# Kernel tuning notes

Measured on AMD Instinct MI355X. Metric: run time of the kernel, lower is better.

## Reference

```python
import jax, jax.numpy as jnp
import numpy as np

# config constants (from init_kwargs)
DT = 1.0
TAU_J = 10.0
TAU_M = 20.0
KAPPA_J = 0.25
A_GEN = 1.0
A_DISC = 1.0
THRESH = 0.4
X_DECAY = 20.0  # trace decay constant: x += -x/20 + spikes

B = 8192
LS = [1024, 512, 512, 256]


def setup_inputs() -> dict:
    key = jax.random.key(0)
    ks = jax.random.split(key, 24)
    inp = {}
    inp['x_input'] = (jax.random.uniform(ks[0], (B, LS[0])) < 0.2).astype(jnp.float32)
    inp['y_target'] = (jax.random.uniform(ks[1], (B, LS[3])) < 0.2).astype(jnp.float32)
    # hidden-layer states (layers 1 and 2); layer 0 / last are clamped
    inp['j1'] = jax.random.normal(ks[2], (B, LS[1])) * 0.1
    inp['v1'] = jax.random.normal(ks[3], (B, LS[1])) * 0.1
    inp['s1'] = (jax.random.uniform(ks[4], (B, LS[1])) < 0.2).astype(jnp.float32)
    inp['x1'] = jax.random.uniform(ks[5], (B, LS[1])) * 2.0
    inp['j2'] = jax.random.normal(ks[6], (B, LS[2])) * 0.1
    inp['v2'] = jax.random.normal(ks[7], (B, LS[2])) * 0.1
    inp['s2'] = (jax.random.uniform(ks[8], (B, LS[2])) < 0.2).astype(jnp.float32)
    inp['x2'] = jax.random.uniform(ks[9], (B, LS[2])) * 2.0
    # weights (torch.rand * 0.01)
    inp['W0'] = jax.random.uniform(ks[10], (LS[0], LS[1])) * 0.01
    inp['W1'] = jax.random.uniform(ks[11], (LS[1], LS[2])) * 0.01
    inp['W2'] = jax.random.uniform(ks[12], (LS[2], LS[3])) * 0.01
    inp['V0'] = jax.random.uniform(ks[13], (LS[1], LS[0])) * 0.01
    inp['V1'] = jax.random.uniform(ks[14], (LS[2], LS[1])) * 0.01
    inp['V2'] = jax.random.uniform(ks[15], (LS[3], LS[2])) * 0.01
    inp['Eg0'] = jax.random.uniform(ks[16], (LS[1], LS[0])) * 0.01
    inp['Eg1'] = jax.random.uniform(ks[17], (LS[2], LS[1])) * 0.01
    inp['Eg2'] = jax.random.uniform(ks[18], (LS[3], LS[2])) * 0.01
    inp['Ed0'] = jax.random.uniform(ks[19], (LS[0], LS[1])) * 0.01
    inp['Ed1'] = jax.random.uniform(ks[20], (LS[1], LS[2])) * 0.01
    inp['Ed2'] = jax.random.uniform(ks[21], (LS[2], LS[3])) * 0.01
    return inp


def _lif_update(j, v, x, total_input):
    # Eq 19-24: leaky current integrator -> leaky membrane -> threshold -> reset -> trace
    j = j + (DT / TAU_J) * (-KAPPA_J * j + total_input)
    v = v + (DT / TAU_M) * (-v + j)  # uses updated j, as in the torch code
    spikes = (v > THRESH).astype(v.dtype)
    v = v * (1.0 - spikes)  # hard reset
    x = x + (-x / X_DECAY + spikes)  # spike trace
    return j, v, spikes, x


def reference(x_input, y_target, j1, v1, s1, x1, j2, v2, s2, x2,
              W0, W1, W2, V0, V1, V2, Eg0, Eg1, Eg2, Ed0, Ed1, Ed2):
    # --- phase 1: error neurons (all layers, using current spikes) ---
    # layer 0 clamped: x0 = x_input, s0 = x_input; layer 3 clamped: x3 = s3 = y_target
    e_gen0 = A_GEN * (x_input - s1 @ W0.T)       # [B, 1024]
    e_gen1 = A_GEN * (x1 - s2 @ W1.T)            # [B, 512]
    e_gen2 = A_GEN * (x2 - y_target @ W2.T)      # [B, 512]
    e_disc1 = A_DISC * (x1 - x_input @ V0.T)     # [B, 512]
    e_disc2 = A_DISC * (x2 - s1 @ V1.T)          # [B, 512]
    e_disc3 = A_DISC * (y_target - s2 @ V2.T)    # [B, 256]

    # --- phase 2: value-neuron updates (hidden layers 1 and 2 only) ---
    total1 = -(e_gen1 + e_disc1) + e_gen0 @ Eg0.T + e_disc2 @ Ed1.T
    total2 = -(e_gen2 + e_disc2) + e_gen1 @ Eg1.T + e_disc3 @ Ed2.T

    j1n, v1n, s1n, x1n = _lif_update(j1, v1, x1, total1)
    j2n, v2n, s2n, x2n = _lif_update(j2, v2, x2, total2)

    return jnp.concatenate([j1n, v1n, x1n, s1n, j2n, v2n, x2n, s2n], axis=-1)  # [B, 4096]
```

## Files before the change

### kernel.cpp

```cpp
#include <hip/hip_runtime.h>
#include <stdint.h>
#include <stddef.h>

typedef unsigned short u16;
typedef __attribute__((ext_vector_type(8))) short short8;
typedef __attribute__((ext_vector_type(4))) float f32x4;

#define DEVI __device__ __forceinline__

DEVI u16 f2bf(float f) {
  union { float f; unsigned u; } c; c.f = f;
  unsigned r = c.u + 0x7fff + ((c.u >> 16) & 1);
  return (u16)(r >> 16);
}

DEVI short8 pack8(f32x4 a, f32x4 b) {
  short8 v;
#pragma unroll
  for (int i = 0; i < 4; i++) { v[i] = (short)f2bf(a[i]); v[i + 4] = (short)f2bf(b[i]); }
  return v;
}

typedef __attribute__((address_space(1))) const void global_cvoid;
typedef __attribute__((address_space(3))) void lds_void;

DEVI void mfma_phase(const u16* As, const u16* Bs, f32x4 acc[4][4])
{
  const int lane = threadIdx.x & 63;
  const int w    = threadIdx.x >> 6;
  const int l16  = lane & 15, lq = lane >> 4;
  const int wm   = (w >> 1) * 64, wn = (w & 1) * 64;
#pragma unroll
  for (int kc = 0; kc < 2; kc++) {
    short8 afr[4], bfr[4];
#pragma unroll
    for (int rt = 0; rt < 4; rt++) {
      int m  = wm + rt * 16 + l16;
      int gr = (kc * 4 + lq) ^ (m & 7);
      afr[rt] = *(const short8*)(As + m * 64 + gr * 8);
    }
#pragma unroll
    for (int ct = 0; ct < 4; ct++) {
      int n  = wn + ct * 16 + l16;
      int gr = (kc * 4 + lq) ^ (n & 7);
      bfr[ct] = *(const short8*)(Bs + n * 64 + gr * 8);
    }
#pragma unroll
    for (int rt = 0; rt < 4; rt++)
#pragma unroll
      for (int ct = 0; ct < 4; ct++)
        acc[rt][ct] = __builtin_amdgcn_mfma_f32_16x16x32_bf16(afr[rt], bfr[ct], acc[rt][ct], 0, 0, 0);
  }
}

DEVI void zero_acc(f32x4 acc[4][4]) {
  f32x4 z = {0.f, 0.f, 0.f, 0.f};
#pragma unroll
  for (int a = 0; a < 4; a++)
#pragma unroll
    for (int b = 0; b < 4; b++) acc[a][b] = z;
}

struct Params {
  const float *x_input, *y_target, *j1, *v1, *s1, *x1, *j2, *v2, *s2, *x2;
  const float *W0, *W1, *W2, *V0, *V1, *V2, *Eg0, *Eg1, *Ed1, *Ed2;
};


DEVI void stage_async(const u16* gbase, int ldr, int k0, u16* lds)
{
  const int t = threadIdx.x;
  const int lane = t & 63, w = t >> 6;
#pragma unroll
  for (int tt = 0; tt < 4; tt++) {
    int rowbase = w * 32 + tt * 8;
    int row = rowbase + (lane >> 3);
    int gsw = (lane & 7) ^ (row & 7);
    __builtin_amdgcn_global_load_lds(
        (global_cvoid*)(gbase + (size_t)row * ldr + k0 + gsw * 8),
        (lds_void*)(lds + rowbase * 64), 16, 0, 0);
  }
}

DEVI void gemm_term_fast(const u16* A, const u16* B, int K,
                         u16* As, u16* Bs, f32x4 acc[4][4])
{
  for (int k0 = 0; k0 < K; k0 += 64) {
    stage_async(A, K, k0, As);
    stage_async(B, K, k0, Bs);
    __syncthreads();
    mfma_phase(As, Bs, acc);
    __syncthreads();
  }
}

struct PJob { const float *s0, *s1; u16* dst; int start; };
struct TJob { const float* in; u16* out; int J, tbase; };
struct PrepArgs { PJob jb[14]; TJob tj[4]; };

__global__ __launch_bounds__(256) void k_prep(PrepArgs A)
{
  __shared__ u16 T[32][33];
  int b = blockIdx.x;
  int t = threadIdx.x;
  if (b < 14464) {
    int ji = 0;
#pragma unroll
    for (int i = 1; i < 14; i++)
      if (b >= A.jb[i].start) ji = i;
    PJob pj = A.jb[ji];
    size_t e0 = ((size_t)(b - pj.start) * 256 + t) * 8;
    const float* s0 = pj.s0 + e0;
    f32x4 a  = *(const f32x4*)s0;
    f32x4 b4 = *(const f32x4*)(s0 + 4);
    if (pj.s1) {
      const float* s1 = pj.s1 + e0;
      a  = a  + *(const f32x4*)s1;
      b4 = b4 + *(const f32x4*)(s1 + 4);
    }
    *(short8*)(pj.dst + e0) = pack8(a, b4);
    return;
  }
  int b2 = b - 14464;
  int ji = 0;
#pragma unroll
  for (int i = 1; i < 4; i++)
    if (b2 >= A.tj[i].tbase) ji = i;
  TJob jb = A.tj[ji];
  int local = b2 - jb.tbase;
  int tm = local >> 4;
  int tk = local & 15;
  int tx = t & 31, ty = t >> 5;
#pragma unroll
  for (int i = 0; i < 4; i++) {
    int r = ty + i * 8;
    T[r][tx] = f2bf(jb.in[(size_t)(tm * 32 + r) * 512 + tk * 32 + tx]);
  }
  __syncthreads();
#pragma unroll
  for (int i = 0; i < 4; i++) {
    int r = ty + i * 8;
    jb.out[(size_t)(tk * 32 + r) * jb.J + tm * 32 + tx] = T[tx][r];
  }
}

struct BW2Args {
  const u16 *Eg0b, *W0tb, *Ed1b, *V1tb, *Eg1b, *W1tb, *Ed2b, *V2tb;
  u16 *Bw1b, *Bw2b;
};

__global__ __launch_bounds__(256) void k_bw2(BW2Args A)
{
  __shared__ u16 As[128 * 64];
  __shared__ u16 Bs[128 * 64];
  int b   = blockIdx.x;
  int mat = b >> 4, loc = b & 15;
  int bmw = loc >> 2, bnw = loc & 3;

  f32x4 acc[4][4];
  zero_acc(acc);
  u16* dst;
  if (mat == 0) {
    gemm_term_fast(A.Eg0b + (size_t)bmw * 128 * 1024, A.W0tb + (size_t)bnw * 128 * 1024, 1024, As, Bs, acc);
    gemm_term_fast(A.Ed1b + (size_t)bmw * 128 * 512,  A.V1tb + (size_t)bnw * 128 * 512,   512, As, Bs, acc);
    dst = A.Bw1b;
  } else {
    gemm_term_fast(A.Eg1b + (size_t)bmw * 128 * 512,  A.W1tb + (size_t)bnw * 128 * 512,   512, As, Bs, acc);
    gemm_term_fast(A.Ed2b + (size_t)bmw * 128 * 256,  A.V2tb + (size_t)bnw * 128 * 256,   256, As, Bs, acc);
    dst = A.Bw2b;
  }
  const int lane = threadIdx.x & 63;
  const int w    = threadIdx.x >> 6;
  const int l16  = lane & 15, lq = lane >> 4;
  const int wm   = (w >> 1) * 64, wn = (w & 1) * 64;
#pragma unroll
  for (int rt = 0; rt < 4; rt++)
#pragma unroll
    for (int ct = 0; ct < 4; ct++)
#pragma unroll
      for (int i = 0; i < 4; i++) {
        int rl = wm + rt * 16 + lq * 4 + i;
        int cl = wn + ct * 16 + l16;
        dst[(size_t)(bmw * 128 + rl) * 512 + bnw * 128 + cl] = f2bf(-acc[rt][ct][i]);
      }
}

struct MJobF {
  const u16* A[4]; const u16* B[4]; int K[4];
  const float *jin, *vin, *xin;
  int obase;
};
struct MArgsF { MJobF j[2]; };

__global__ __launch_bounds__(256) void k_main_fast(MArgsF P, float* __restrict__ out)
{
  __shared__ u16 As[128 * 64];
  __shared__ u16 Bs[128 * 64];
  int job   = blockIdx.x >> 8;
  int local = blockIdx.x & 255;
  int bm = local & 63, bn = local >> 6;
  MJobF jb = P.j[job];

  f32x4 acc[4][4];
  zero_acc(acc);
#pragma unroll
  for (int p = 0; p < 4; p++)
    gemm_term_fast(jb.A[p] + (size_t)bm * 128 * jb.K[p],
                   jb.B[p] + (size_t)bn * 128 * jb.K[p], jb.K[p], As, Bs, acc);

  const int lane = threadIdx.x & 63;
  const int w    = threadIdx.x >> 6;
  const int l16  = lane & 15, lq = lane >> 4;
  const int wm   = (w >> 1) * 64, wn = (w & 1) * 64;

#pragma unroll
  for (int rt = 0; rt < 4; rt++)
#pragma unroll
    for (int ct = 0; ct < 4; ct++)
#pragma unroll
      for (int i = 0; i < 4; i++) {
        int row    = bm * 128 + wm + rt * 16 + lq * 4 + i;
        int col    = bn * 128 + wn + ct * 16 + l16;
        size_t idx = (size_t)row * 512 + col;
        float xf = jb.xin[idx];
        float total = acc[rt][ct][i] - 2.0f * xf;
        float jf = jb.jin[idx];
        float vf = jb.vin[idx];
        jf = jf + 0.1f * (-0.25f * jf + total);
        vf = vf + 0.05f * (-vf + jf);
        float sf = (vf > 0.4f) ? 1.0f : 0.0f;
        vf = vf * (1.0f - sf);
        xf = xf + (-xf / 20.0f + sf);
        size_t ob = (size_t)row * 4096 + jb.obase + col;
        out[ob]        = jf;
        out[ob + 512]  = vf;
        out[ob + 1024] = xf;
        out[ob + 1536] = sf;
      }
}


DEVI void stage_A_fb(const float* A, int ldr, int k0, u16* dst)
{
  const int t = threadIdx.x;
  const int g = t & 7, rb = t >> 3;
#pragma unroll
  for (int p = 0; p < 4; p++) {
    int row = p * 32 + rb;
    const float* src = A + (size_t)row * ldr + k0 + g * 8;
    f32x4 a = *(const f32x4*)src;
    f32x4 b = *(const f32x4*)(src + 4);
    *(short8*)(dst + row * 64 + (g ^ (row & 7)) * 8) = pack8(a, b);
  }
}

DEVI void nn_term_fb(const float* A, const float* B, int K, u16* As, u16* Bs, f32x4 acc[4][4])
{
  const int t  = threadIdx.x;
  const int ks = t >> 4, ng = t & 15;
  for (int k0 = 0; k0 < K; k0 += 64) {
    stage_A_fb(A, K, k0, As);
#pragma unroll
    for (int i = 0; i < 4; i++) {
      int kloc = i * 16 + ks;
      const float* src = B + (size_t)(k0 + kloc) * 512 + ng * 8;
      f32x4 a = *(const f32x4*)src;
      f32x4 b = *(const f32x4*)(src + 4);
#pragma unroll
      for (int e = 0; e < 8; e++) {
        int nloc = ng * 8 + e;
        float val = (e < 4) ? a[e] : b[e - 4];
        Bs[nloc * 64 + ((kloc >> 3) ^ (nloc & 7)) * 8 + (kloc & 7)] = f2bf(val);
      }
    }
    __syncthreads();
    mfma_phase(As, Bs, acc);
    __syncthreads();
  }
}

template <int MODE>
DEVI void gemm_term_fb(const float* A, const float* B0, const float* B1, int K,
                       u16* As, u16* Bs, f32x4 acc[4][4])
{
  const int t = threadIdx.x;
  const int g = t & 7, rb = t >> 3;
  for (int k0 = 0; k0 < K; k0 += 64) {
    stage_A_fb(A, K, k0, As);
#pragma unroll
    for (int p = 0; p < 4; p++) {
      int row = p * 32 + rb;
      const float* src;
      if (MODE == 2) src = B0 + (size_t)row * 4096 + (k0 >> 7) * 512 + (k0 & 127) + g * 8;
      else           src = B0 + (size_t)row * K + k0 + g * 8;
      f32x4 a = *(const f32x4*)src;
      f32x4 b = *(const f32x4*)(src + 4);
      if (MODE == 1) {
        const float* s2 = B1 + (size_t)row * K + k0 + g * 8;
        a = a + *(const f32x4*)s2;
        b = b + *(const f32x4*)(s2 + 4);
      }
      *(short8*)(Bs + row * 64 + (g ^ (row & 7)) * 8) = pack8(a, b);
    }
    __syncthreads();
    mfma_phase(As, Bs, acc);
    __syncthreads();
  }
}

__global__ __launch_bounds__(256) void k_bw_fb(Params P, float* __restrict__ out)
{
  __shared__ u16 As[128 * 64];
  __shared__ u16 Bs[128 * 64];
  int b   = blockIdx.x;
  int mat = b >> 4, loc = b & 15;
  int bmw = loc >> 2, bnw = loc & 3;

  f32x4 acc[4][4];
  zero_acc(acc);
  int obase;
  if (mat == 0) {
    nn_term_fb(P.Eg0 + (size_t)bmw * 128 * 1024, P.W0 + bnw * 128, 1024, As, Bs, acc);
    nn_term_fb(P.Ed1 + (size_t)bmw * 128 * 512,  P.V1 + bnw * 128,  512, As, Bs, acc);
    obase = 0;
  } else {
    nn_term_fb(P.Eg1 + (size_t)bmw * 128 * 512,  P.W1 + bnw * 128,  512, As, Bs, acc);
    nn_term_fb(P.Ed2 + (size_t)bmw * 128 * 256,  P.V2 + bnw * 128,  256, As, Bs, acc);
    obase = 2048;
  }
  const int lane = threadIdx.x & 63;
  const int w    = threadIdx.x >> 6;
  const int l16  = lane & 15, lq = lane >> 4;
  const int wm   = (w >> 1) * 64, wn = (w & 1) * 64;
#pragma unroll
  for (int rt = 0; rt < 4; rt++)
#pragma unroll
    for (int ct = 0; ct < 4; ct++)
#pragma unroll
      for (int i = 0; i < 4; i++) {
        int rl = wm + rt * 16 + lq * 4 + i;
        int cl = wn + ct * 16 + l16;
        out[(size_t)rl * 4096 + obase + bmw * 128 + bnw * 512 + cl] = -acc[rt][ct][i];
      }
}

__global__ __launch_bounds__(256) void k_main_fb(Params P, float* __restrict__ out, int fix)
{
  __shared__ u16 As[128 * 64];
  __shared__ u16 Bs[128 * 64];
  int job, bm, bn;
  if (fix) {
    job = blockIdx.x >> 2; bn = blockIdx.x & 3; bm = 0;
  } else {
    job = blockIdx.x >> 8;
    int local = blockIdx.x & 255;
    bm = local & 63; bn = local >> 6;
    if (bm == 0) return;
  }

  f32x4 acc[4][4];
  zero_acc(acc);
  const float *jin, *vin, *xin;
  int obase;
  size_t am = (size_t)bm * 128;

  if (job == 0) {
    gemm_term_fb<0>(P.s2      + am * 512,  P.W1  + (size_t)bn * 128 * 512,  nullptr, 512,  As, Bs, acc);
    gemm_term_fb<1>(P.x_input + am * 1024, P.V0  + (size_t)bn * 128 * 1024,
                    P.Eg0 + (size_t)bn * 128 * 1024, 1024, As, Bs, acc);
    gemm_term_fb<0>(P.x2      + am * 512,  P.Ed1 + (size_t)bn * 128 * 512,  nullptr, 512,  As, Bs, acc);
    gemm_term_fb<2>(P.s1      + am * 512,  out + 0 + bn * 128,              nullptr, 512,  As, Bs, acc);
    jin = P.j1; vin = P.v1; xin = P.x1; obase = 0;
  } else {
    gemm_term_fb<1>(P.y_target + am * 256, P.W2  + (size_t)bn * 128 * 256,
                    P.Ed2 + (size_t)bn * 128 * 256, 256, As, Bs, acc);
    gemm_term_fb<0>(P.s1      + am * 512,  P.V1  + (size_t)bn * 128 * 512,  nullptr, 512,  As, Bs, acc);
    gemm_term_fb<0>(P.x1      + am * 512,  P.Eg1 + (size_t)bn * 128 * 512,  nullptr, 512,  As, Bs, acc);
    gemm_term_fb<2>(P.s2      + am * 512,  out + 2048 + bn * 128,           nullptr, 512,  As, Bs, acc);
    jin = P.j2; vin = P.v2; xin = P.x2; obase = 2048;
  }

  const int lane = threadIdx.x & 63;
  const int w    = threadIdx.x >> 6;
  const int l16  = lane & 15, lq = lane >> 4;
  const int wm   = (w >> 1) * 64, wn = (w & 1) * 64;

#pragma unroll
  for (int rt = 0; rt < 4; rt++)
#pragma unroll
    for (int ct = 0; ct < 4; ct++)
#pragma unroll
      for (int i = 0; i < 4; i++) {
        int row    = bm * 128 + wm + rt * 16 + lq * 4 + i;
        int col    = bn * 128 + wn + ct * 16 + l16;
        size_t idx = (size_t)row * 512 + col;
        float xf = xin[idx];
        float total = acc[rt][ct][i] - 2.0f * xf;
        float jf = jin[idx];
        float vf = vin[idx];
        jf = jf + 0.1f * (-0.25f * jf + total);
        vf = vf + 0.05f * (-vf + jf);
        float sf = (vf > 0.4f) ? 1.0f : 0.0f;
        vf = vf * (1.0f - sf);
        xf = xf + (-xf / 20.0f + sf);
        size_t ob = (size_t)row * 4096 + obase + col;
        out[ob]        = jf;
        out[ob + 512]  = vf;
        out[ob + 1024] = xf;
        out[ob + 1536] = sf;
      }
}

extern "C" void kernel_launch(void* const* d_in, const int* in_sizes, int n_in,
                              void* d_out, int out_size, void* d_ws, size_t ws_size,
                              hipStream_t stream)
{
  Params P;
  P.x_input  = (const float*)d_in[0];
  P.y_target = (const float*)d_in[1];
  P.j1 = (const float*)d_in[2];
  P.v1 = (const float*)d_in[3];
  P.s1 = (const float*)d_in[4];
  P.x1 = (const float*)d_in[5];
  P.j2 = (const float*)d_in[6];
  P.v2 = (const float*)d_in[7];
  P.s2 = (const float*)d_in[8];
  P.x2 = (const float*)d_in[9];
  P.W0 = (const float*)d_in[10];
  P.W1 = (const float*)d_in[11];
  P.W2 = (const float*)d_in[12];
  P.V0 = (const float*)d_in[13];
  P.V1 = (const float*)d_in[14];
  P.V2 = (const float*)d_in[15];
  P.Eg0 = (const float*)d_in[16];
  P.Eg1 = (const float*)d_in[17];
  P.Ed1 = (const float*)d_in[20];
  P.Ed2 = (const float*)d_in[21];
  (void)in_sizes; (void)n_in; (void)out_size;

  float* out = (float*)d_out;

  if (ws_size >= 62652416) {
    char* ws = (char*)d_ws;
    u16* xin_b = (u16*)(ws + 0);
    u16* y_b   = (u16*)(ws + 16777216);
    u16* s1_b  = (u16*)(ws + 20971520);
    u16* x1_b  = (u16*)(ws + 29360128);
    u16* s2_b  = (u16*)(ws + 37748736);
    u16* x2_b  = (u16*)(ws + 46137344);
    u16* W1_b  = (u16*)(ws + 54525952);
    u16* P1_b  = (u16*)(ws + 55050240);
    u16* Ed1_b = (u16*)(ws + 56098816);
    u16* V1_b  = (u16*)(ws + 56623104);
    u16* Eg1_b = (u16*)(ws + 57147392);
    u16* P2_b  = (u16*)(ws + 57671680);
    u16* Bw1_b = (u16*)(ws + 57933824);
    u16* Bw2_b = (u16*)(ws + 58458112);
    u16* W0t_b = (u16*)(ws + 58982400);
    u16* V1t_b = (u16*)(ws + 60030976);
    u16* W1t_b = (u16*)(ws + 60555264);
    u16* V2t_b = (u16*)(ws + 61079552);
    u16* Eg0_b = (u16*)(ws + 61341696);
    u16* Ed2_b = (u16*)(ws + 62390272);

    PrepArgs pa;
    pa.jb[0]  = { P.x_input,  nullptr, xin_b,     0 };
    pa.jb[1]  = { P.y_target, nullptr, y_b,    4096 };
    pa.jb[2]  = { P.s1,       nullptr, s1_b,   5120 };
    pa.jb[3]  = { P.x1,       nullptr, x1_b,   7168 };
    pa.jb[4]  = { P.s2,       nullptr, s2_b,   9216 };
    pa.jb[5]  = { P.x2,       nullptr, x2_b,  11264 };
    pa.jb[6]  = { P.W1,       nullptr, W1_b,  13312 };
    pa.jb[7]  = { P.V0,       P.Eg0,   P1_b,  13440 };
    pa.jb[8]  = { P.Ed1,      nullptr, Ed1_b, 13696 };
    pa.jb[9]  = { P.V1,       nullptr, V1_b,  13824 };
    pa.jb[10] = { P.Eg1,      nullptr, Eg1_b, 13952 };
    pa.jb[11] = { P.W2,       P.Ed2,   P2_b,  14080 };
    pa.jb[12] = { P.Eg0,      nullptr, Eg0_b, 14144 };
    pa.jb[13] = { P.Ed2,      nullptr, Ed2_b, 14400 };
    pa.tj[0]  = { P.W0, W0t_b, 1024,    0 };
    pa.tj[1]  = { P.V1, V1t_b,  512,  512 };
    pa.tj[2]  = { P.W1, W1t_b,  512,  768 };
    pa.tj[3]  = { P.V2, V2t_b,  256, 1024 };
    k_prep<<<dim3(15616), dim3(256), 0, stream>>>(pa);

    BW2Args ba;
    ba.Eg0b = Eg0_b; ba.W0tb = W0t_b; ba.Ed1b = Ed1_b; ba.V1tb = V1t_b;
    ba.Eg1b = Eg1_b; ba.W1tb = W1t_b; ba.Ed2b = Ed2_b; ba.V2tb = V2t_b;
    ba.Bw1b = Bw1_b; ba.Bw2b = Bw2_b;
    k_bw2<<<dim3(32), dim3(256), 0, stream>>>(ba);

    MArgsF ma;
    ma.j[0].A[0] = s2_b;  ma.j[0].B[0] = W1_b;  ma.j[0].K[0] = 512;
    ma.j[0].A[1] = xin_b; ma.j[0].B[1] = P1_b;  ma.j[0].K[1] = 1024;
    ma.j[0].A[2] = x2_b;  ma.j[0].B[2] = Ed1_b; ma.j[0].K[2] = 512;
    ma.j[0].A[3] = s1_b;  ma.j[0].B[3] = Bw1_b; ma.j[0].K[3] = 512;
    ma.j[0].jin = P.j1; ma.j[0].vin = P.v1; ma.j[0].xin = P.x1; ma.j[0].obase = 0;
    ma.j[1].A[0] = y_b;   ma.j[1].B[0] = P2_b;  ma.j[1].K[0] = 256;
    ma.j[1].A[1] = s1_b;  ma.j[1].B[1] = V1_b;  ma.j[1].K[1] = 512;
    ma.j[1].A[2] = x1_b;  ma.j[1].B[2] = Eg1_b; ma.j[1].K[2] = 512;
    ma.j[1].A[3] = s2_b;  ma.j[1].B[3] = Bw2_b; ma.j[1].K[3] = 512;
    ma.j[1].jin = P.j2; ma.j[1].vin = P.v2; ma.j[1].xin = P.x2; ma.j[1].obase = 2048;
    k_main_fast<<<dim3(512), dim3(256), 0, stream>>>(ma, out);
  } else {
    k_bw_fb<<<dim3(32), dim3(256), 0, stream>>>(P, out);
    k_main_fb<<<dim3(512), dim3(256), 0, stream>>>(P, out, 0);
    k_main_fb<<<dim3(8), dim3(256), 0, stream>>>(P, out, 1);
  }
}
```

Measured before the change: 414.2 us.

## Merge prep and weight-product kernels; halve main GEMM M-tile for more blocks

The separate transpose and bf16-weight-product kernels are folded into one pre-kernel. Its first 32 blocks compute the Bw1/Bw2 weight products directly from fp32 weights with the NN fallback path, and the remaining blocks convert four chunks each. This removes one launch, the transposed weight copies and the Eg0/Ed2 bf16 copies. The main fused GEMM now uses 64-row tiles with 1024 blocks and a launch bound of 4 to raise occupancy on 256 CUs. The cost is more B-tile reloads per output and a slower fp32-sourced weight-product path that runs alongside the conversion blocks.

```diff
diff --git a/kernel.cpp b/kernel.cpp
--- a/kernel.cpp
+++ b/kernel.cpp
@@ -24,6 +24,7 @@
 typedef __attribute__((address_space(1))) const void global_cvoid;
 typedef __attribute__((address_space(3))) void lds_void;
 
+
 DEVI void mfma_phase(const u16* As, const u16* Bs, f32x4 acc[4][4])
 {
   const int lane = threadIdx.x & 63;
@@ -53,10 +54,47 @@
   }
 }
 
+DEVI void mfma_phase64(const u16* As, const u16* Bs, f32x4 acc[2][4])
+{
+  const int lane = threadIdx.x & 63;
+  const int w    = threadIdx.x >> 6;
+  const int l16  = lane & 15, lq = lane >> 4;
+  const int wm   = (w >> 1) * 32, wn = (w & 1) * 64;
+#pragma unroll
+  for (int kc = 0; kc < 2; kc++) {
+    short8 afr[2], bfr[4];
+#pragma unroll
+    for (int rt = 0; rt < 2; rt++) {
+      int m  = wm + rt * 16 + l16;
+      int gr = (kc * 4 + lq) ^ (m & 7);
+      afr[rt] = *(const short8*)(As + m * 64 + gr * 8);
+    }
+#pragma unroll
+    for (int ct = 0; ct < 4; ct++) {
+      int n  = wn + ct * 16 + l16;
+      int gr = (kc * 4 + lq) ^ (n & 7);
+      bfr[ct] = *(const short8*)(Bs + n * 64 + gr * 8);
+    }
+#pragma unroll
+    for (int rt = 0; rt < 2; rt++)
+#pragma unroll
+      for (int ct = 0; ct < 4; ct++)
+        acc[rt][ct] = __builtin_amdgcn_mfma_f32_16x16x32_bf16(afr[rt], bfr[ct], acc[rt][ct], 0, 0, 0);
+  }
+}
+
 DEVI void zero_acc(f32x4 acc[4][4]) {
   f32x4 z = {0.f, 0.f, 0.f, 0.f};
 #pragma unroll
   for (int a = 0; a < 4; a++)
+#pragma unroll
+    for (int b = 0; b < 4; b++) acc[a][b] = z;
+}
+
+DEVI void zero_acc24(f32x4 acc[2][4]) {
+  f32x4 z = {0.f, 0.f, 0.f, 0.f};
+#pragma unroll
+  for (int a = 0; a < 2; a++)
 #pragma unroll
     for (int b = 0; b < 4; b++) acc[a][b] = z;
 }
@@ -67,13 +105,14 @@
 };
 
 
+template <int RR>
 DEVI void stage_async(const u16* gbase, int ldr, int k0, u16* lds)
 {
   const int t = threadIdx.x;
   const int lane = t & 63, w = t >> 6;
 #pragma unroll
-  for (int tt = 0; tt < 4; tt++) {
-    int rowbase = w * 32 + tt * 8;
+  for (int tt = 0; tt < RR; tt++) {
+    int rowbase = w * (RR * 8) + tt * 8;
     int row = rowbase + (lane >> 3);
     int gsw = (lane & 7) ^ (row & 7);
     __builtin_amdgcn_global_load_lds(
@@ -82,12 +121,51 @@
   }
 }
 
-DEVI void gemm_term_fast(const u16* A, const u16* B, int K,
-                         u16* As, u16* Bs, f32x4 acc[4][4])
+DEVI void gemm_term_main(const u16* A, const u16* B, int K,
+                         u16* As, u16* Bs, f32x4 acc[2][4])
 {
   for (int k0 = 0; k0 < K; k0 += 64) {
-    stage_async(A, K, k0, As);
-    stage_async(B, K, k0, Bs);
+    stage_async<2>(A, K, k0, As);
+    stage_async<4>(B, K, k0, Bs);
+    __syncthreads();
+    mfma_phase64(As, Bs, acc);
+    __syncthreads();
+  }
+}
+
+DEVI void stage_A_fb(const float* A, int ldr, int k0, u16* dst)
+{
+  const int t = threadIdx.x;
+  const int g = t & 7, rb = t >> 3;
+#pragma unroll
+  for (int p = 0; p < 4; p++) {
+    int row = p * 32 + rb;
+    const float* src = A + (size_t)row * ldr + k0 + g * 8;
+    f32x4 a = *(const f32x4*)src;
+    f32x4 b = *(const f32x4*)(src + 4);
+    *(short8*)(dst + row * 64 + (g ^ (row & 7)) * 8) = pack8(a, b);
+  }
+}
+
+DEVI void nn_term_fb(const float* A, const float* B, int K, u16* As, u16* Bs, f32x4 acc[4][4])
+{
+  const int t  = threadIdx.x;
+  const int ks = t >> 4, ng = t & 15;
+  for (int k0 = 0; k0 < K; k0 += 64) {
+    stage_A_fb(A, K, k0, As);
+#pragma unroll
+    for (int i = 0; i < 4; i++) {
+      int kloc = i * 16 + ks;
+      const float* src = B + (size_t)(k0 + kloc) * 512 + ng * 8;
+      f32x4 a = *(const f32x4*)src;
+      f32x4 b = *(const f32x4*)(src + 4);
+#pragma unroll
+      for (int e = 0; e < 8; e++) {
+        int nloc = ng * 8 + e;
+        float val = (e < 4) ? a[e] : b[e - 4];
+        Bs[nloc * 64 + ((kloc >> 3) ^ (nloc & 7)) * 8 + (kloc & 7)] = f2bf(val);
+      }
+    }
     __syncthreads();
     mfma_phase(As, Bs, acc);
     __syncthreads();
@@ -95,21 +173,60 @@
 }
 
 struct PJob { const float *s0, *s1; u16* dst; int start; };
-struct TJob { const float* in; u16* out; int J, tbase; };
-struct PrepArgs { PJob jb[14]; TJob tj[4]; };
-
-__global__ __launch_bounds__(256) void k_prep(PrepArgs A)
-{
-  __shared__ u16 T[32][33];
+struct PreArgs {
+  const float *W0, *V1, *W1, *V2, *Eg0, *Ed1, *Eg1, *Ed2;
+  u16 *Bw1b, *Bw2b;
+  PJob jb[12];
+};
+
+__global__ __launch_bounds__(256) void k_pre(PreArgs A)
+{
+  __shared__ u16 As[128 * 64];
+  __shared__ u16 Bs[128 * 64];
   int b = blockIdx.x;
   int t = threadIdx.x;
-  if (b < 14464) {
+
+  if (b < 32) {
+    int mat = b >> 4, loc = b & 15;
+    int bmw = loc >> 2, bnw = loc & 3;
+    f32x4 acc[4][4];
+    zero_acc(acc);
+    u16* dst;
+    if (mat == 0) {
+      nn_term_fb(A.Eg0 + (size_t)bmw * 128 * 1024, A.W0 + bnw * 128, 1024, As, Bs, acc);
+      nn_term_fb(A.Ed1 + (size_t)bmw * 128 * 512,  A.V1 + bnw * 128,  512, As, Bs, acc);
+      dst = A.Bw1b;
+    } else {
+      nn_term_fb(A.Eg1 + (size_t)bmw * 128 * 512,  A.W1 + bnw * 128,  512, As, Bs, acc);
+      nn_term_fb(A.Ed2 + (size_t)bmw * 128 * 256,  A.V2 + bnw * 128,  256, As, Bs, acc);
+      dst = A.Bw2b;
+    }
+    const int lane = t & 63;
+    const int w    = t >> 6;
+    const int l16  = lane & 15, lq = lane >> 4;
+    const int wm   = (w >> 1) * 64, wn = (w & 1) * 64;
+#pragma unroll
+    for (int rt = 0; rt < 4; rt++)
+#pragma unroll
+      for (int ct = 0; ct < 4; ct++)
+#pragma unroll
+        for (int i = 0; i < 4; i++) {
+          int rl = wm + rt * 16 + lq * 4 + i;
+          int cl = wn + ct * 16 + l16;
+          dst[(size_t)(bmw * 128 + rl) * 512 + bnw * 128 + cl] = f2bf(-acc[rt][ct][i]);
+        }
+    return;
+  }
+
+  int cb = (b - 32) * 4;
+  for (int it = 0; it < 4; it++) {
+    int c = cb + it;
     int ji = 0;
 #pragma unroll
-    for (int i = 1; i < 14; i++)
-      if (b >= A.jb[i].start) ji = i;
+    for (int i = 1; i < 12; i++)
+      if (c >= A.jb[i].start) ji = i;
     PJob pj = A.jb[ji];
-    size_t e0 = ((size_t)(b - pj.start) * 256 + t) * 8;
+    size_t e0 = ((size_t)(c - pj.start) * 256 + t) * 8;
     const float* s0 = pj.s0 + e0;
     f32x4 a  = *(const f32x4*)s0;
     f32x4 b4 = *(const f32x4*)(s0 + 4);
@@ -119,70 +236,7 @@
       b4 = b4 + *(const f32x4*)(s1 + 4);
     }
     *(short8*)(pj.dst + e0) = pack8(a, b4);
-    return;
-  }
-  int b2 = b - 14464;
-  int ji = 0;
-#pragma unroll
-  for (int i = 1; i < 4; i++)
-    if (b2 >= A.tj[i].tbase) ji = i;
-  TJob jb = A.tj[ji];
-  int local = b2 - jb.tbase;
-  int tm = local >> 4;
-  int tk = local & 15;
-  int tx = t & 31, ty = t >> 5;
-#pragma unroll
-  for (int i = 0; i < 4; i++) {
-    int r = ty + i * 8;
-    T[r][tx] = f2bf(jb.in[(size_t)(tm * 32 + r) * 512 + tk * 32 + tx]);
-  }
-  __syncthreads();
-#pragma unroll
-  for (int i = 0; i < 4; i++) {
-    int r = ty + i * 8;
-    jb.out[(size_t)(tk * 32 + r) * jb.J + tm * 32 + tx] = T[tx][r];
-  }
-}
-
-struct BW2Args {
-  const u16 *Eg0b, *W0tb, *Ed1b, *V1tb, *Eg1b, *W1tb, *Ed2b, *V2tb;
-  u16 *Bw1b, *Bw2b;
-};
-
-__global__ __launch_bounds__(256) void k_bw2(BW2Args A)
-{
-  __shared__ u16 As[128 * 64];
-  __shared__ u16 Bs[128 * 64];
-  int b   = blockIdx.x;
-  int mat = b >> 4, loc = b & 15;
-  int bmw = loc >> 2, bnw = loc & 3;
-
-  f32x4 acc[4][4];
-  zero_acc(acc);
-  u16* dst;
-  if (mat == 0) {
-    gemm_term_fast(A.Eg0b + (size_t)bmw * 128 * 1024, A.W0tb + (size_t)bnw * 128 * 1024, 1024, As, Bs, acc);
-    gemm_term_fast(A.Ed1b + (size_t)bmw * 128 * 512,  A.V1tb + (size_t)bnw * 128 * 512,   512, As, Bs, acc);
-    dst = A.Bw1b;
-  } else {
-    gemm_term_fast(A.Eg1b + (size_t)bmw * 128 * 512,  A.W1tb + (size_t)bnw * 128 * 512,   512, As, Bs, acc);
-    gemm_term_fast(A.Ed2b + (size_t)bmw * 128 * 256,  A.V2tb + (size_t)bnw * 128 * 256,   256, As, Bs, acc);
-    dst = A.Bw2b;
-  }
-  const int lane = threadIdx.x & 63;
-  const int w    = threadIdx.x >> 6;
-  const int l16  = lane & 15, lq = lane >> 4;
-  const int wm   = (w >> 1) * 64, wn = (w & 1) * 64;
-#pragma unroll
-  for (int rt = 0; rt < 4; rt++)
-#pragma unroll
-    for (int ct = 0; ct < 4; ct++)
-#pragma unroll
-      for (int i = 0; i < 4; i++) {
-        int rl = wm + rt * 16 + lq * 4 + i;
-        int cl = wn + ct * 16 + l16;
-        dst[(size_t)(bmw * 128 + rl) * 512 + bnw * 128 + cl] = f2bf(-acc[rt][ct][i]);
-      }
+  }
 }
 
 struct MJobF {
@@ -192,34 +246,34 @@
 };
 struct MArgsF { MJobF j[2]; };
 
-__global__ __launch_bounds__(256) void k_main_fast(MArgsF P, float* __restrict__ out)
-{
-  __shared__ u16 As[128 * 64];
+__global__ __launch_bounds__(256, 4) void k_main_fast(MArgsF P, float* __restrict__ out)
+{
+  __shared__ u16 As[64 * 64];
   __shared__ u16 Bs[128 * 64];
-  int job   = blockIdx.x >> 8;
-  int local = blockIdx.x & 255;
-  int bm = local & 63, bn = local >> 6;
+  int job   = blockIdx.x >> 9;
+  int local = blockIdx.x & 511;
+  int bm = local & 127, bn = local >> 7;
   MJobF jb = P.j[job];
 
-  f32x4 acc[4][4];
-  zero_acc(acc);
+  f32x4 acc[2][4];
+  zero_acc24(acc);
 #pragma unroll
   for (int p = 0; p < 4; p++)
-    gemm_term_fast(jb.A[p] + (size_t)bm * 128 * jb.K[p],
+    gemm_term_main(jb.A[p] + (size_t)bm * 64 * jb.K[p],
                    jb.B[p] + (size_t)bn * 128 * jb.K[p], jb.K[p], As, Bs, acc);
 
   const int lane = threadIdx.x & 63;
   const int w    = threadIdx.x >> 6;
   const int l16  = lane & 15, lq = lane >> 4;
-  const int wm   = (w >> 1) * 64, wn = (w & 1) * 64;
-
-#pragma unroll
-  for (int rt = 0; rt < 4; rt++)
+  const int wm   = (w >> 1) * 32, wn = (w & 1) * 64;
+
+#pragma unroll
+  for (int rt = 0; rt < 2; rt++)
 #pragma unroll
     for (int ct = 0; ct < 4; ct++)
 #pragma unroll
       for (int i = 0; i < 4; i++) {
-        int row    = bm * 128 + wm + rt * 16 + lq * 4 + i;
+        int row    = bm * 64 + wm + rt * 16 + lq * 4 + i;
         int col    = bn * 128 + wn + ct * 16 + l16;
         size_t idx = (size_t)row * 512 + col;
         float xf = jb.xin[idx];
@@ -239,45 +293,6 @@
       }
 }
 
-
-DEVI void stage_A_fb(const float* A, int ldr, int k0, u16* dst)
-{
-  const int t = threadIdx.x;
-  const int g = t & 7, rb = t >> 3;
-#pragma unroll
-  for (int p = 0; p < 4; p++) {
-    int row = p * 32 + rb;
-    const float* src = A + (size_t)row * ldr + k0 + g * 8;
-    f32x4 a = *(const f32x4*)src;
-    f32x4 b = *(const f32x4*)(src + 4);
-    *(short8*)(dst + row * 64 + (g ^ (row & 7)) * 8) = pack8(a, b);
-  }
-}
-
-DEVI void nn_term_fb(const float* A, const float* B, int K, u16* As, u16* Bs, f32x4 acc[4][4])
-{
-  const int t  = threadIdx.x;
-  const int ks = t >> 4, ng = t & 15;
-  for (int k0 = 0; k0 < K; k0 += 64) {
-    stage_A_fb(A, K, k0, As);
-#pragma unroll
-    for (int i = 0; i < 4; i++) {
-      int kloc = i * 16 + ks;
-      const float* src = B + (size_t)(k0 + kloc) * 512 + ng * 8;
-      f32x4 a = *(const f32x4*)src;
-      f32x4 b = *(const f32x4*)(src + 4);
-#pragma unroll
-      for (int e = 0; e < 8; e++) {
-        int nloc = ng * 8 + e;
-        float val = (e < 4) ? a[e] : b[e - 4];
-        Bs[nloc * 64 + ((kloc >> 3) ^ (nloc & 7)) * 8 + (kloc & 7)] = f2bf(val);
-      }
-    }
-    __syncthreads();
-    mfma_phase(As, Bs, acc);
-    __syncthreads();
-  }
-}
 
 template <int MODE>
 DEVI void gemm_term_fb(const float* A, const float* B0, const float* B1, int K,
@@ -440,7 +455,7 @@
 
   float* out = (float*)d_out;
 
-  if (ws_size >= 62652416) {
+  if (ws_size >= 58982400) {
     char* ws = (char*)d_ws;
     u16* xin_b = (u16*)(ws + 0);
     u16* y_b   = (u16*)(ws + 16777216);
@@ -456,14 +471,11 @@
     u16* P2_b  = (u16*)(ws + 57671680);
     u16* Bw1_b = (u16*)(ws + 57933824);
     u16* Bw2_b = (u16*)(ws + 58458112);
-    u16* W0t_b = (u16*)(ws + 58982400);
-    u16* V1t_b = (u16*)(ws + 60030976);
-    u16* W1t_b = (u16*)(ws + 60555264);
-    u16* V2t_b = (u16*)(ws + 61079552);
-    u16* Eg0_b = (u16*)(ws + 61341696);
-    u16* Ed2_b = (u16*)(ws + 62390272);
-
-    PrepArgs pa;
+
+    PreArgs pa;
+    pa.W0 = P.W0; pa.V1 = P.V1; pa.W1 = P.W1; pa.V2 = P.V2;
+    pa.Eg0 = P.Eg0; pa.Ed1 = P.Ed1; pa.Eg1 = P.Eg1; pa.Ed2 = P.Ed2;
+    pa.Bw1b = Bw1_b; pa.Bw2b = Bw2_b;
     pa.jb[0]  = { P.x_input,  nullptr, xin_b,     0 };
     pa.jb[1]  = { P.y_target, nullptr, y_b,    4096 };
     pa.jb[2]  = { P.s1,       nullptr, s1_b,   5120 };
@@ -476,19 +488,7 @@
     pa.jb[9]  = { P.V1,       nullptr, V1_b,  13824 };
     pa.jb[10] = { P.Eg1,      nullptr, Eg1_b, 13952 };
     pa.jb[11] = { P.W2,       P.Ed2,   P2_b,  14080 };
-    pa.jb[12] = { P.Eg0,      nullptr, Eg0_b, 14144 };
-    pa.jb[13] = { P.Ed2,      nullptr, Ed2_b, 14400 };
-    pa.tj[0]  = { P.W0, W0t_b, 1024,    0 };
-    pa.tj[1]  = { P.V1, V1t_b,  512,  512 };
-    pa.tj[2]  = { P.W1, W1t_b,  512,  768 };
-    pa.tj[3]  = { P.V2, V2t_b,  256, 1024 };
-    k_prep<<<dim3(15616), dim3(256), 0, stream>>>(pa);
-
-    BW2Args ba;
-    ba.Eg0b = Eg0_b; ba.W0tb = W0t_b; ba.Ed1b = Ed1_b; ba.V1tb = V1t_b;
-    ba.Eg1b = Eg1_b; ba.W1tb = W1t_b; ba.Ed2b = Ed2_b; ba.V2tb = V2t_b;
-    ba.Bw1b = Bw1_b; ba.Bw2b = Bw2_b;
-    k_bw2<<<dim3(32), dim3(256), 0, stream>>>(ba);
+    k_pre<<<dim3(3568), dim3(256), 0, stream>>>(pa);
 
     MArgsF ma;
     ma.j[0].A[0] = s2_b;  ma.j[0].B[0] = W1_b;  ma.j[0].K[0] = 512;
@@ -501,7 +501,7 @@
     ma.j[1].A[2] = x1_b;  ma.j[1].B[2] = Eg1_b; ma.j[1].K[2] = 512;
     ma.j[1].A[3] = s2_b;  ma.j[1].B[3] = Bw2_b; ma.j[1].K[3] = 512;
     ma.j[1].jin = P.j2; ma.j[1].vin = P.v2; ma.j[1].xin = P.x2; ma.j[1].obase = 2048;
-    k_main_fast<<<dim3(512), dim3(256), 0, stream>>>(ma, out);
+    k_main_fast<<<dim3(1024), dim3(256), 0, stream>>>(ma, out);
   } else {
     k_bw_fb<<<dim3(32), dim3(256), 0, stream>>>(P, out);
     k_main_fb<<<dim3(512), dim3(256), 0, stream>>>(P, out, 0);
```

After: 451.2 us. +8.9%, slower.

## Double-buffer LDS loads and halve M tile in main fused GEMM kernel

Applied to the files above, without the earlier changes.

The main GEMM+LIF kernel now uses 64x128 tiles instead of 128x128, doubling the grid to 1024 blocks. It also double-buffers the A and B tiles in LDS, using vmcnt waits so the next K slice's async global-to-LDS loads overlap MFMA work on the current one. This targets the load-then-compute stalls of the single-buffered loop and the low block count on a large GPU. The cost is more LDS per block, a lower launch-bounds occupancy hint, and lower per-block arithmetic intensity from the smaller M tile.

```diff
diff --git a/kernel.cpp b/kernel.cpp
--- a/kernel.cpp
+++ b/kernel.cpp
@@ -24,6 +24,7 @@
 typedef __attribute__((address_space(1))) const void global_cvoid;
 typedef __attribute__((address_space(3))) void lds_void;
 
+
 DEVI void mfma_phase(const u16* As, const u16* Bs, f32x4 acc[4][4])
 {
   const int lane = threadIdx.x & 63;
@@ -53,10 +54,47 @@
   }
 }
 
+DEVI void mfma_phase64(const u16* As, const u16* Bs, f32x4 acc[2][4])
+{
+  const int lane = threadIdx.x & 63;
+  const int w    = threadIdx.x >> 6;
+  const int l16  = lane & 15, lq = lane >> 4;
+  const int wm   = (w >> 1) * 32, wn = (w & 1) * 64;
+#pragma unroll
+  for (int kc = 0; kc < 2; kc++) {
+    short8 afr[2], bfr[4];
+#pragma unroll
+    for (int rt = 0; rt < 2; rt++) {
+      int m  = wm + rt * 16 + l16;
+      int gr = (kc * 4 + lq) ^ (m & 7);
+      afr[rt] = *(const short8*)(As + m * 64 + gr * 8);
+    }
+#pragma unroll
+    for (int ct = 0; ct < 4; ct++) {
+      int n  = wn + ct * 16 + l16;
+      int gr = (kc * 4 + lq) ^ (n & 7);
+      bfr[ct] = *(const short8*)(Bs + n * 64 + gr * 8);
+    }
+#pragma unroll
+    for (int rt = 0; rt < 2; rt++)
+#pragma unroll
+      for (int ct = 0; ct < 4; ct++)
+        acc[rt][ct] = __builtin_amdgcn_mfma_f32_16x16x32_bf16(afr[rt], bfr[ct], acc[rt][ct], 0, 0, 0);
+  }
+}
+
 DEVI void zero_acc(f32x4 acc[4][4]) {
   f32x4 z = {0.f, 0.f, 0.f, 0.f};
 #pragma unroll
   for (int a = 0; a < 4; a++)
+#pragma unroll
+    for (int b = 0; b < 4; b++) acc[a][b] = z;
+}
+
+DEVI void zero_acc24(f32x4 acc[2][4]) {
+  f32x4 z = {0.f, 0.f, 0.f, 0.f};
+#pragma unroll
+  for (int a = 0; a < 2; a++)
 #pragma unroll
     for (int b = 0; b < 4; b++) acc[a][b] = z;
 }
@@ -67,13 +105,14 @@
 };
 
 
+template <int RR>
 DEVI void stage_async(const u16* gbase, int ldr, int k0, u16* lds)
 {
   const int t = threadIdx.x;
   const int lane = t & 63, w = t >> 6;
 #pragma unroll
-  for (int tt = 0; tt < 4; tt++) {
-    int rowbase = w * 32 + tt * 8;
+  for (int tt = 0; tt < RR; tt++) {
+    int rowbase = w * (RR * 8) + tt * 8;
     int row = rowbase + (lane >> 3);
     int gsw = (lane & 7) ^ (row & 7);
     __builtin_amdgcn_global_load_lds(
@@ -86,11 +125,36 @@
                          u16* As, u16* Bs, f32x4 acc[4][4])
 {
   for (int k0 = 0; k0 < K; k0 += 64) {
-    stage_async(A, K, k0, As);
-    stage_async(B, K, k0, Bs);
+    stage_async<4>(A, K, k0, As);
+    stage_async<4>(B, K, k0, Bs);
     __syncthreads();
     mfma_phase(As, Bs, acc);
     __syncthreads();
+  }
+}
+
+DEVI void gemm_term_pipe(const u16* A, const u16* B, int K,
+                         u16* As0, u16* As1, u16* Bs0, u16* Bs1, f32x4 acc[2][4])
+{
+  const int nt = K >> 6;
+  stage_async<2>(A, K, 0, As0);
+  stage_async<4>(B, K, 0, Bs0);
+  stage_async<2>(A, K, 64, As1);
+  stage_async<4>(B, K, 64, Bs1);
+  for (int t = 0; t < nt; t++) {
+    if (t < nt - 1) asm volatile("s_waitcnt vmcnt(6)" ::: "memory");
+    else            asm volatile("s_waitcnt vmcnt(0)" ::: "memory");
+    __builtin_amdgcn_s_barrier();
+    __builtin_amdgcn_sched_barrier(0);
+    if (t & 1) mfma_phase64(As1, Bs1, acc);
+    else       mfma_phase64(As0, Bs0, acc);
+    asm volatile("s_waitcnt lgkmcnt(0)" ::: "memory");
+    __builtin_amdgcn_sched_barrier(0);
+    __builtin_amdgcn_s_barrier();
+    if (t + 2 < nt) {
+      if (t & 1) { stage_async<2>(A, K, (t + 2) * 64, As1); stage_async<4>(B, K, (t + 2) * 64, Bs1); }
+      else       { stage_async<2>(A, K, (t + 2) * 64, As0); stage_async<4>(B, K, (t + 2) * 64, Bs0); }
+    }
   }
 }
 
@@ -192,34 +256,37 @@
 };
 struct MArgsF { MJobF j[2]; };
 
-__global__ __launch_bounds__(256) void k_main_fast(MArgsF P, float* __restrict__ out)
-{
-  __shared__ u16 As[128 * 64];
-  __shared__ u16 Bs[128 * 64];
-  int job   = blockIdx.x >> 8;
-  int local = blockIdx.x & 255;
-  int bm = local & 63, bn = local >> 6;
+__global__ __launch_bounds__(256, 3) void k_main_fast(MArgsF P, float* __restrict__ out)
+{
+  __shared__ __align__(16) u16 As0[64 * 64];
+  __shared__ __align__(16) u16 As1[64 * 64];
+  __shared__ __align__(16) u16 Bs0[128 * 64];
+  __shared__ __align__(16) u16 Bs1[128 * 64];
+  int job   = blockIdx.x >> 9;
+  int local = blockIdx.x & 511;
+  int bm = local & 127, bn = local >> 7;
   MJobF jb = P.j[job];
 
-  f32x4 acc[4][4];
-  zero_acc(acc);
+  f32x4 acc[2][4];
+  zero_acc24(acc);
 #pragma unroll
   for (int p = 0; p < 4; p++)
-    gemm_term_fast(jb.A[p] + (size_t)bm * 128 * jb.K[p],
-                   jb.B[p] + (size_t)bn * 128 * jb.K[p], jb.K[p], As, Bs, acc);
+    gemm_term_pipe(jb.A[p] + (size_t)bm * 64 * jb.K[p],
+                   jb.B[p] + (size_t)bn * 128 * jb.K[p], jb.K[p],
+                   As0, As1, Bs0, Bs1, acc);
 
   const int lane = threadIdx.x & 63;
   const int w    = threadIdx.x >> 6;
   const int l16  = lane & 15, lq = lane >> 4;
-  const int wm   = (w >> 1) * 64, wn = (w & 1) * 64;
-
-#pragma unroll
-  for (int rt = 0; rt < 4; rt++)
+  const int wm   = (w >> 1) * 32, wn = (w & 1) * 64;
+
+#pragma unroll
+  for (int rt = 0; rt < 2; rt++)
 #pragma unroll
     for (int ct = 0; ct < 4; ct++)
 #pragma unroll
       for (int i = 0; i < 4; i++) {
-        int row    = bm * 128 + wm + rt * 16 + lq * 4 + i;
+        int row    = bm * 64 + wm + rt * 16 + lq * 4 + i;
         int col    = bn * 128 + wn + ct * 16 + l16;
         size_t idx = (size_t)row * 512 + col;
         float xf = jb.xin[idx];
@@ -501,7 +568,7 @@
     ma.j[1].A[2] = x1_b;  ma.j[1].B[2] = Eg1_b; ma.j[1].K[2] = 512;
     ma.j[1].A[3] = s2_b;  ma.j[1].B[3] = Bw2_b; ma.j[1].K[3] = 512;
     ma.j[1].jin = P.j2; ma.j[1].vin = P.v2; ma.j[1].xin = P.x2; ma.j[1].obase = 2048;
-    k_main_fast<<<dim3(512), dim3(256), 0, stream>>>(ma, out);
+    k_main_fast<<<dim3(1024), dim3(256), 0, stream>>>(ma, out);
   } else {
     k_bw_fb<<<dim3(32), dim3(256), 0, stream>>>(P, out);
     k_main_fb<<<dim3(512), dim3(256), 0, stream>>>(P, out, 0);
```

Measured after the change: 433.0 us. 1.05x slower.
